# Kernel tuning notes

Hardware: AMD Instinct MI355X
Metric: run time of the kernel (lower is better)

Reference implementation:

```python
import jax, jax.numpy as jnp
import numpy as np
from jax import lax


def setup_inputs() -> dict:
    key = jax.random.key(0)
    k1, k2, k3, k4 = jax.random.split(key, 4)
    N, D, B, R, EF = 100000, 256, 64, 32, 32
    storage = jax.random.normal(k1, (N, D), dtype=jnp.float32)
    query = jax.random.normal(k2, (B, D), dtype=jnp.float32)
    graph = jax.random.randint(k3, (N, R), 0, N, dtype=jnp.int32)      # fixed-degree NSW adjacency
    initial = jax.random.randint(k4, (B, EF), 0, N, dtype=jnp.int32)   # random entry points (entry())
    return {"query": query, "storage": storage, "graph": graph,
            "initial": initial, "k": 10, "ef_search": EF}


def reference(query, storage, graph, initial, k, ef_search):
    """Batched greedy best-first NSW search (ef_search fixed expansion steps)."""
    N = storage.shape[0]
    INF = jnp.float32(1e30)

    def sqdist(q, ids):
        diff = storage[ids] - q            # [R, D] gather
        return jnp.sum(diff * diff, axis=-1)

    def search_one(q, init):
        cd = sqdist(q, init)                               # candidate distances [EF]
        visited = jnp.zeros((N,), jnp.bool_).at[init].set(True)
        expanded = jnp.zeros((N,), jnp.bool_)

        def step(state, _):
            cid, cd, visited, expanded = state
            # pick closest unexpanded candidate
            pickd = jnp.where(expanded[cid], INF, cd)
            j = jnp.argmin(pickd)
            u = cid[j]
            expanded = expanded.at[u].set(True)
            # expand neighbors of u
            nbrs = graph[u]                                # [R]
            fresh = ~visited[nbrs]
            nd = jnp.where(fresh, sqdist(q, nbrs), INF)    # skip already-visited
            visited = visited.at[nbrs].set(True)
            # merge candidate pool, keep ef_search best
            all_ids = jnp.concatenate([cid, nbrs])
            all_d = jnp.concatenate([cd, nd])
            negd, idx = lax.top_k(-all_d, ef_search)
            return (all_ids[idx], -negd, visited, expanded), None

        (cid, cd, _, _), _ = lax.scan(step, (init, cd, visited, expanded),
                                      None, length=ef_search)
        negk, idx = lax.top_k(-cd, k)
        return cid[idx], -negk

    topk_ids, topk_dists = jax.vmap(search_one)(query, initial)
    return topk_ids, topk_dists
```

## Files before the change

### kernel.cpp

```cpp
#include <hip/hip_runtime.h>


#define DIMS   256
#define RDEG   32
#define EFPOOL 32
#define KOUT   10
#define NWORDS 3125
#define INF_D  1e30f

__global__ __launch_bounds__(64, 1) void nsw_wave_kernel(
    const float* __restrict__ query,
    const float* __restrict__ storage,
    const int*   __restrict__ graph,
    const int*   __restrict__ initial,
    float*       __restrict__ out,
    int B)
{
    __shared__ unsigned int visited[NWORDS];
    __shared__ unsigned int expanded[NWORDS];
    __shared__ float4 qsh[DIMS / 4];
    __shared__ unsigned long long keys[64];
    __shared__ float sc_d[EFPOOL];
    __shared__ int   sc_id[EFPOOL];

    const int l    = threadIdx.x;
    const int b    = blockIdx.x;
    const int nb   = l & 31;
    const int half = l >> 5;

    for (int i = l; i < NWORDS; i += 64) { visited[i] = 0u; expanded[i] = 0u; }

    qsh[l] = reinterpret_cast<const float4*>(query + (size_t)b * DIMS)[l];

    float pool_d  = INF_D;
    int   pool_id = 0;
    int   u;

    auto merge_pick = [&](float nd, int nbid) {
        float ed  = half ? nd   : pool_d;
        int   eid = half ? nbid : pool_id;
        unsigned long long key =
            ((unsigned long long)__float_as_uint(ed) << 6) | (unsigned)l;
        keys[l] = key;
        int rank = 0;
        #pragma unroll
        for (int j = 0; j < 64; ++j)
            rank += (keys[j] < key) ? 1 : 0;
        if (rank < EFPOOL) { sc_d[rank] = ed; sc_id[rank] = eid; }
        pool_d  = sc_d[nb];
        pool_id = sc_id[nb];
        bool unexp = !((expanded[pool_id >> 5] >> (pool_id & 31)) & 1u);
        unsigned long long m = __ballot(unexp && (l < 32));
        int slot = (m == 0ull) ? 0 : (__ffsll((unsigned long long)m) - 1);
        u = sc_id[slot];
        if (l == 0) expanded[u >> 5] |= (1u << (u & 31));
    };

    {
        int nbid = initial[b * EFPOOL + nb];
        const float4* sp = reinterpret_cast<const float4*>(storage + (size_t)nbid * DIMS) + half * 32;
        float4 r[32];
        #pragma unroll
        for (int j = 0; j < 32; ++j) r[j] = sp[j];
        if (l < 32) atomicOr(&visited[nbid >> 5], 1u << (nbid & 31));
        float a0 = 0.f, a1 = 0.f, a2 = 0.f, a3 = 0.f;
        #pragma unroll
        for (int j = 0; j < 32; ++j) {
            float4 q = qsh[half * 32 + j];
            float d0 = r[j].x - q.x; a0 = fmaf(d0, d0, a0);
            float d1 = r[j].y - q.y; a1 = fmaf(d1, d1, a1);
            float d2 = r[j].z - q.z; a2 = fmaf(d2, d2, a2);
            float d3 = r[j].w - q.w; a3 = fmaf(d3, d3, a3);
        }
        float part = (a0 + a1) + (a2 + a3);
        float nd = part + __shfl_xor(part, 32, 64);
        merge_pick(nd, nbid);
    }

    for (int step = 0; step < EFPOOL; ++step) {
        int nbid = graph[(size_t)u * RDEG + nb];
        const float4* sp = reinterpret_cast<const float4*>(storage + (size_t)nbid * DIMS) + half * 32;
        float4 r[32];
        #pragma unroll
        for (int j = 0; j < 32; ++j) r[j] = sp[j];

        unsigned vw = visited[nbid >> 5];
        bool fresh = !((vw >> (nbid & 31)) & 1u);
        if ((l < 32) && fresh) atomicOr(&visited[nbid >> 5], 1u << (nbid & 31));

        float a0 = 0.f, a1 = 0.f, a2 = 0.f, a3 = 0.f;
        #pragma unroll
        for (int j = 0; j < 32; ++j) {
            float4 q = qsh[half * 32 + j];
            float d0 = r[j].x - q.x; a0 = fmaf(d0, d0, a0);
            float d1 = r[j].y - q.y; a1 = fmaf(d1, d1, a1);
            float d2 = r[j].z - q.z; a2 = fmaf(d2, d2, a2);
            float d3 = r[j].w - q.w; a3 = fmaf(d3, d3, a3);
        }
        float part = (a0 + a1) + (a2 + a3);
        float d = part + __shfl_xor(part, 32, 64);
        float nd = fresh ? d : INF_D;

        merge_pick(nd, nbid);
    }

    if (l < KOUT) {
        out[b * KOUT + l]            = (float)pool_id;
        out[B * KOUT + b * KOUT + l] = pool_d;
    }
}

extern "C" void kernel_launch(void* const* d_in, const int* in_sizes, int n_in,
                              void* d_out, int out_size, void* d_ws, size_t ws_size,
                              hipStream_t stream) {
    const float* query   = (const float*)d_in[0];
    const float* storage = (const float*)d_in[1];
    const int*   graph   = (const int*)d_in[2];
    const int*   initial = (const int*)d_in[3];
    float* out = (float*)d_out;

    const int B = in_sizes[0] / DIMS;

    nsw_wave_kernel<<<B, 64, 0, stream>>>(query, storage, graph, initial, out, B);
}
```

Baseline: 233.5 us.

## Stage neighbor rows via async LDS loads and speculatively prefetch next adjacency row

```diff
diff --git a/kernel.cpp b/kernel.cpp
--- a/kernel.cpp
+++ b/kernel.cpp
@@ -7,6 +7,8 @@
 #define KOUT   10
 #define NWORDS 3125
 #define INF_D  1e30f
+
+typedef unsigned long long u64;
 
 __global__ __launch_bounds__(64, 1) void nsw_wave_kernel(
     const float* __restrict__ query,
@@ -19,14 +21,16 @@
     __shared__ unsigned int visited[NWORDS];
     __shared__ unsigned int expanded[NWORDS];
     __shared__ float4 qsh[DIMS / 4];
-    __shared__ unsigned long long keys[64];
-    __shared__ float sc_d[EFPOOL];
-    __shared__ int   sc_id[EFPOOL];
+    __shared__ float  rows[RDEG * DIMS];
+    __shared__ u64    keys[64];
+    __shared__ float  sc_d[EFPOOL];
+    __shared__ int    sc_id[EFPOOL];
 
     const int l    = threadIdx.x;
     const int b    = blockIdx.x;
     const int nb   = l & 31;
     const int half = l >> 5;
+    const int sw   = nb & 7;
 
     for (int i = l; i < NWORDS; i += 64) { visited[i] = 0u; expanded[i] = 0u; }
 
@@ -34,74 +38,89 @@
 
     float pool_d  = INF_D;
     int   pool_id = 0;
-    int   u;
+    int   u       = 0;
+    int   nbid    = initial[b * EFPOOL + nb];
 
-    auto merge_pick = [&](float nd, int nbid) {
-        float ed  = half ? nd   : pool_d;
-        int   eid = half ? nbid : pool_id;
-        unsigned long long key =
-            ((unsigned long long)__float_as_uint(ed) << 6) | (unsigned)l;
-        keys[l] = key;
-        int rank = 0;
+    for (int s = 0; s <= EFPOOL; ++s) {
+        const bool is_init = (s == 0);
+
+        if (!is_init && l == 0) expanded[u >> 5] |= 1u << (u & 31);
+
         #pragma unroll
-        for (int j = 0; j < 64; ++j)
-            rank += (keys[j] < key) ? 1 : 0;
-        if (rank < EFPOOL) { sc_d[rank] = ed; sc_id[rank] = eid; }
-        pool_d  = sc_d[nb];
-        pool_id = sc_id[nb];
-        bool unexp = !((expanded[pool_id >> 5] >> (pool_id & 31)) & 1u);
-        unsigned long long m = __ballot(unexp && (l < 32));
-        int slot = (m == 0ull) ? 0 : (__ffsll((unsigned long long)m) - 1);
-        u = sc_id[slot];
-        if (l == 0) expanded[u >> 5] |= (1u << (u & 31));
-    };
+        for (int j = 0; j < RDEG; ++j) {
+            int gidj = __shfl(nbid, j, 64);
+            const float* src = storage + (size_t)gidj * DIMS + ((l ^ (j & 7)) << 2);
+            __builtin_amdgcn_global_load_lds(
+                (const __attribute__((address_space(1))) void*)src,
+                (__attribute__((address_space(3))) void*)&rows[j * DIMS], 16, 0, 0);
+        }
 
-    {
-        int nbid = initial[b * EFPOOL + nb];
-        const float4* sp = reinterpret_cast<const float4*>(storage + (size_t)nbid * DIMS) + half * 32;
-        float4 r[32];
-        #pragma unroll
-        for (int j = 0; j < 32; ++j) r[j] = sp[j];
-        if (l < 32) atomicOr(&visited[nbid >> 5], 1u << (nbid & 31));
+        unsigned vw = visited[nbid >> 5];
+        bool fresh = is_init ? true : !((vw >> (nbid & 31)) & 1u);
+        if ((l < 32) && fresh) atomicOr(&visited[nbid >> 5], 1u << (nbid & 31));
+
+        asm volatile("s_waitcnt vmcnt(0)" ::: "memory");
         float a0 = 0.f, a1 = 0.f, a2 = 0.f, a3 = 0.f;
-        #pragma unroll
-        for (int j = 0; j < 32; ++j) {
-            float4 q = qsh[half * 32 + j];
-            float d0 = r[j].x - q.x; a0 = fmaf(d0, d0, a0);
-            float d1 = r[j].y - q.y; a1 = fmaf(d1, d1, a1);
-            float d2 = r[j].z - q.z; a2 = fmaf(d2, d2, a2);
-            float d3 = r[j].w - q.w; a3 = fmaf(d3, d3, a3);
+        {
+            const float4* rp = reinterpret_cast<const float4*>(rows) + nb * 64 + half * 32;
+            const float4* qp = qsh + half * 32;
+            #pragma unroll
+            for (int j = 0; j < 32; ++j) {
+                float4 r = rp[j ^ sw];
+                float4 q = qp[j];
+                float d0 = r.x - q.x; a0 = fmaf(d0, d0, a0);
+                float d1 = r.y - q.y; a1 = fmaf(d1, d1, a1);
+                float d2 = r.z - q.z; a2 = fmaf(d2, d2, a2);
+                float d3 = r.w - q.w; a3 = fmaf(d3, d3, a3);
+            }
         }
         float part = (a0 + a1) + (a2 + a3);
-        float nd = part + __shfl_xor(part, 32, 64);
-        merge_pick(nd, nbid);
-    }
-
-    for (int step = 0; step < EFPOOL; ++step) {
-        int nbid = graph[(size_t)u * RDEG + nb];
-        const float4* sp = reinterpret_cast<const float4*>(storage + (size_t)nbid * DIMS) + half * 32;
-        float4 r[32];
-        #pragma unroll
-        for (int j = 0; j < 32; ++j) r[j] = sp[j];
-
-        unsigned vw = visited[nbid >> 5];
-        bool fresh = !((vw >> (nbid & 31)) & 1u);
-        if ((l < 32) && fresh) atomicOr(&visited[nbid >> 5], 1u << (nbid & 31));
-
-        float a0 = 0.f, a1 = 0.f, a2 = 0.f, a3 = 0.f;
-        #pragma unroll
-        for (int j = 0; j < 32; ++j) {
-            float4 q = qsh[half * 32 + j];
-            float d0 = r[j].x - q.x; a0 = fmaf(d0, d0, a0);
-            float d1 = r[j].y - q.y; a1 = fmaf(d1, d1, a1);
-            float d2 = r[j].z - q.z; a2 = fmaf(d2, d2, a2);
-            float d3 = r[j].w - q.w; a3 = fmaf(d3, d3, a3);
-        }
-        float part = (a0 + a1) + (a2 + a3);
-        float d = part + __shfl_xor(part, 32, 64);
+        float d  = part + __shfl_xor(part, 32, 64);
         float nd = fresh ? d : INF_D;
 
-        merge_pick(nd, nbid);
+        bool eflag = half ? (!fresh)
+                          : (((expanded[pool_id >> 5] >> (pool_id & 31)) & 1u) != 0u);
+        float ed_e = half ? nd : pool_d;
+        u64 ek = ((u64)(eflag ? 1u : 0u) << 62)
+               | ((u64)__float_as_uint(ed_e) << 6) | (unsigned)l;
+        #pragma unroll
+        for (int m = 1; m < 64; m <<= 1) {
+            u64 o = __shfl_xor(ek, m, 64);
+            ek = (o < ek) ? o : ek;
+        }
+        int cidx  = (int)(ek & 63);
+        int myid  = half ? nbid : pool_id;
+        int uspec = __shfl(myid, cidx, 64);
+
+        int nnbid = graph[(size_t)uspec * RDEG + nb];
+
+        {
+            float ed  = half ? nd   : pool_d;
+            int   eid = half ? nbid : pool_id;
+            u64 key = ((u64)__float_as_uint(ed) << 6) | (unsigned)l;
+            keys[l] = key;
+            int rank = 0;
+            #pragma unroll
+            for (int j = 0; j < 64; ++j)
+                rank += (keys[j] < key) ? 1 : 0;
+            if (rank < EFPOOL) { sc_d[rank] = ed; sc_id[rank] = eid; }
+            pool_d  = sc_d[nb];
+            pool_id = sc_id[nb];
+        }
+
+        {
+            bool unexp = !((expanded[pool_id >> 5] >> (pool_id & 31)) & 1u);
+            u64 bm = __ballot(unexp && (l < 32));
+            int slot = (bm == 0ull) ? 0 : (__ffsll(bm) - 1);
+            int utrue = sc_id[slot];
+            int ut = __builtin_amdgcn_readfirstlane(utrue);
+            int us = __builtin_amdgcn_readfirstlane(uspec);
+            if (ut != us) {
+                nnbid = graph[(size_t)ut * RDEG + nb];
+            }
+            u = utrue;
+        }
+        nbid = nnbid;
     }
 
     if (l < KOUT) {
```

Result: slower. 260.0 us (+11.3%).
